# Kernel tuning notes

Measured on AMD Instinct MI355X. Metric: run time of the kernel, lower is better.

The kernel has to match this reference:

```python
import jax, jax.numpy as jnp
import numpy as np

N_NODES = 100000
N_EDGES = 1600000
D = 128
D_FF = 2 * D
BN_EPS = 1e-5


def setup_inputs() -> dict:
    key = jax.random.key(0)
    ks = jax.random.split(key, 16)
    s = lambda k, shp, fan: jax.random.normal(k, shp, jnp.float32) / np.float32(np.sqrt(fan))
    return {
        "x": jax.random.normal(ks[0], (N_NODES, D), jnp.float32),
        "edge_attr": jax.random.normal(ks[1], (N_EDGES, D), jnp.float32),
        "w1g": s(ks[2], (D, D), D),
        "b1g": jnp.zeros((D,), jnp.float32),
        "w2g": s(ks[3], (D, D), D),
        "b2g": jnp.zeros((D,), jnp.float32),
        "bn1_g": jax.random.uniform(ks[4], (D,), jnp.float32, 0.5, 1.5),
        "bn1_b": 0.1 * jax.random.normal(ks[5], (D,), jnp.float32),
        "ff_w1": s(ks[6], (D, D_FF), D),
        "ff_b1": jnp.zeros((D_FF,), jnp.float32),
        "ff_w2": s(ks[7], (D_FF, D), D_FF),
        "ff_b2": jnp.zeros((D,), jnp.float32),
        "bn2_g": jax.random.uniform(ks[8], (D,), jnp.float32, 0.5, 1.5),
        "bn2_b": 0.1 * jax.random.normal(ks[9], (D,), jnp.float32),
        "edge_index": jax.random.randint(ks[10], (2, N_EDGES), 0, N_NODES, jnp.int64 if jax.config.jax_enable_x64 else jnp.int32),
    }


def _batchnorm(h, gamma, beta):
    # training-mode BatchNorm1d: per-batch (node-axis) stats, biased variance
    mean = h.mean(axis=0)
    var = ((h - mean) ** 2).mean(axis=0)
    return gamma * (h - mean) * jax.lax.rsqrt(var + BN_EPS) + beta


def reference(x, edge_attr, w1g, b1g, w2g, b2g, bn1_g, bn1_b,
              ff_w1, ff_b1, ff_w2, ff_b2, bn2_g, bn2_b, edge_index):
    src, dst = edge_index[0], edge_index[1]
    # GINEConv message: relu(x_j + e_ij), scatter-sum into target nodes
    msg = jax.nn.relu(x[src] + edge_attr)                      # [E, D]
    agg = jax.ops.segment_sum(msg, dst, num_segments=N_NODES)  # [N, D]
    h = x + agg                                                # (1+eps)*x with eps=0
    # gin_nn: Linear -> ReLU -> Linear
    h = jax.nn.relu(h @ w1g + b1g) @ w2g + b2g
    h = jax.nn.relu(h)                                         # post-conv relu; dropout=identity (eval)
    h = x + h                                                  # residual
    h = _batchnorm(h, bn1_g, bn1_b)                            # norm1_local
    ff = jax.nn.relu(h @ ff_w1 + ff_b1) @ ff_w2 + ff_b2        # FFN block (dropouts identity)
    h = h + ff
    h = _batchnorm(h, bn2_g, bn2_b)                            # norm2
    return h
```

## Files before the change

### kernel.cpp

```cpp
#include <hip/hip_runtime.h>
#include <hip/hip_bf16.h>

#define NN 100000
#define NE 1600000
#define DD 128
#define DFF 256
#define BN_EPS 1e-5f
#define NND ((size_t)NN * DD)
#define NB_SCAN 391
#define NTILE 6250

typedef __attribute__((ext_vector_type(8))) short short8;
typedef __attribute__((ext_vector_type(4))) float f32x4;
typedef __attribute__((ext_vector_type(4))) unsigned short us4;

static __device__ __forceinline__ unsigned short f2bf(float f) {
  union { float f; unsigned u; } v; v.f = f;
  unsigned r = v.u + 0x7fffu + ((v.u >> 16) & 1u);
  return (unsigned short)(r >> 16);
}
static __device__ __forceinline__ float bf2f(unsigned short h) {
  union { unsigned u; float f; } v; v.u = ((unsigned)h) << 16;
  return v.f;
}

__global__ __launch_bounds__(256) void k_prep_misc(const float* __restrict__ x,
    unsigned short* __restrict__ xbf,
    const float* __restrict__ w1g, const float* __restrict__ w2g,
    const float* __restrict__ ffw1, const float* __restrict__ ffw2,
    unsigned short* __restrict__ w1t, unsigned short* __restrict__ w2t,
    unsigned short* __restrict__ fw1t, unsigned short* __restrict__ fw2t) {
  int b = blockIdx.x;
  if (b < 6250) {
    size_t base = ((size_t)b * 256u + threadIdx.x) * 8;
    const f32x4* xp = reinterpret_cast<const f32x4*>(x + base);
    f32x4 a0 = xp[0], a1 = xp[1];
    short8 o;
#pragma unroll
    for (int j = 0; j < 4; ++j) o[j] = (short)f2bf(a0[j]);
#pragma unroll
    for (int j = 0; j < 4; ++j) o[4 + j] = (short)f2bf(a1[j]);
    *reinterpret_cast<short8*>(xbf + base) = o;
  } else {
    int i = (b - 6250) * 256 + threadIdx.x;
    if (i < 16384) { int c = i & 127, k = i >> 7; w1t[c * 128 + k] = f2bf(w1g[k * 128 + c]); }
    else if (i < 32768) { i -= 16384; int c = i & 127, k = i >> 7; w2t[c * 128 + k] = f2bf(w2g[k * 128 + c]); }
    else if (i < 65536) { i -= 32768; int c = i & 255, k = i >> 8; fw1t[c * 128 + k] = f2bf(ffw1[k * 256 + c]); }
    else if (i < 98304) { i -= 65536; int c = i & 127, k = i >> 7; fw2t[c * 256 + k] = f2bf(ffw2[k * 128 + c]); }
  }
}

__global__ __launch_bounds__(256) void k_hist(const int* __restrict__ ei,
                                              int* __restrict__ cnt) {
  int e = blockIdx.x * 256 + threadIdx.x;
  if (e >= NE) return;
  atomicAdd(&cnt[ei[NE + e]], 1);
}

__global__ __launch_bounds__(256) void k_scan1(const int* __restrict__ cnt,
                                               int* __restrict__ bsum) {
  __shared__ int sh[256];
  int n = blockIdx.x * 256 + threadIdx.x;
  sh[threadIdx.x] = (n < NN) ? cnt[n] : 0;
  __syncthreads();
  for (int off = 128; off > 0; off >>= 1) {
    if (threadIdx.x < off) sh[threadIdx.x] += sh[threadIdx.x + off];
    __syncthreads();
  }
  if (threadIdx.x == 0) bsum[blockIdx.x] = sh[0];
}

__global__ __launch_bounds__(512) void k_scan2(const int* __restrict__ bsum,
                                               int* __restrict__ bpre,
                                               int* __restrict__ rs) {
  __shared__ int sh[512];
  int t = threadIdx.x;
  int v = (t < NB_SCAN) ? bsum[t] : 0;
  sh[t] = v;
  __syncthreads();
  for (int off = 1; off < 512; off <<= 1) {
    int u = (t >= off) ? sh[t - off] : 0;
    __syncthreads();
    sh[t] += u;
    __syncthreads();
  }
  if (t < NB_SCAN) bpre[t] = sh[t] - v;
  if (t == NB_SCAN - 1) rs[NN] = sh[t];
}

__global__ __launch_bounds__(256) void k_scan3(int* __restrict__ rs,
                                               const int* __restrict__ bpre,
                                               int* __restrict__ cursor) {
  __shared__ int sh[256];
  int n = blockIdx.x * 256 + threadIdx.x;
  int t = threadIdx.x;
  int v = (n < NN) ? rs[n] : 0;
  sh[t] = v;
  __syncthreads();
  for (int off = 1; off < 256; off <<= 1) {
    int u = (t >= off) ? sh[t - off] : 0;
    __syncthreads();
    sh[t] += u;
    __syncthreads();
  }
  if (n < NN) {
    int ex = bpre[blockIdx.x] + sh[t] - v;
    rs[n] = ex;
    cursor[n] = ex;
  }
}

__global__ __launch_bounds__(256) void k_scatter(const int* __restrict__ ei,
                                                 int* __restrict__ cursor,
                                                 int2* __restrict__ el2) {
  int e = blockIdx.x * 256 + threadIdx.x;
  if (e >= NE) return;
  int s = ei[e], d = ei[NE + e];
  int p = atomicAdd(&cursor[d], 1);
  el2[p] = make_int2(e, s);
}

__global__ __launch_bounds__(256) void k_gather(
    const unsigned short* __restrict__ xbf, const float* __restrict__ ea,
    const int* __restrict__ rs, const int2* __restrict__ el2,
    unsigned short* __restrict__ h0) {
  int n = blockIdx.x * 8 + (threadIdx.x >> 5);
  int q = threadIdx.x & 31;
  int beg = rs[n], end = rs[n + 1];
  f32x4 acc = (f32x4){0.f, 0.f, 0.f, 0.f};
  int2 E0 = make_int2(0, 0), E1 = E0, E2 = E0, E3 = E0;
  int i = beg;
  if (i     < end) E0 = el2[i];
  if (i + 1 < end) E1 = el2[i + 1];
  if (i + 2 < end) E2 = el2[i + 2];
  if (i + 3 < end) E3 = el2[i + 3];
  for (; i + 4 <= end; i += 4) {
    f32x4 ev0 = *(reinterpret_cast<const f32x4*>(ea + (size_t)E0.x * DD) + q);
    us4  xv0 = *reinterpret_cast<const us4*>(xbf + (size_t)E0.y * DD + q * 4);
    f32x4 ev1 = *(reinterpret_cast<const f32x4*>(ea + (size_t)E1.x * DD) + q);
    us4  xv1 = *reinterpret_cast<const us4*>(xbf + (size_t)E1.y * DD + q * 4);
    f32x4 ev2 = *(reinterpret_cast<const f32x4*>(ea + (size_t)E2.x * DD) + q);
    us4  xv2 = *reinterpret_cast<const us4*>(xbf + (size_t)E2.y * DD + q * 4);
    f32x4 ev3 = *(reinterpret_cast<const f32x4*>(ea + (size_t)E3.x * DD) + q);
    us4  xv3 = *reinterpret_cast<const us4*>(xbf + (size_t)E3.y * DD + q * 4);
    int2 N0 = E0, N1 = E1, N2 = E2, N3 = E3;
    if (i + 4 < end) N0 = el2[i + 4];
    if (i + 5 < end) N1 = el2[i + 5];
    if (i + 6 < end) N2 = el2[i + 6];
    if (i + 7 < end) N3 = el2[i + 7];
#pragma unroll
    for (int c = 0; c < 4; ++c) {
      float m0 = bf2f((unsigned short)xv0[c]) + ev0[c];
      acc[c] += (m0 > 0.f) ? m0 : 0.f;
      float m1 = bf2f((unsigned short)xv1[c]) + ev1[c];
      acc[c] += (m1 > 0.f) ? m1 : 0.f;
      float m2 = bf2f((unsigned short)xv2[c]) + ev2[c];
      acc[c] += (m2 > 0.f) ? m2 : 0.f;
      float m3 = bf2f((unsigned short)xv3[c]) + ev3[c];
      acc[c] += (m3 > 0.f) ? m3 : 0.f;
    }
    E0 = N0; E1 = N1; E2 = N2; E3 = N3;
  }
  if (i < end) {
    f32x4 ev = *(reinterpret_cast<const f32x4*>(ea + (size_t)E0.x * DD) + q);
    us4  xv = *reinterpret_cast<const us4*>(xbf + (size_t)E0.y * DD + q * 4);
#pragma unroll
    for (int c = 0; c < 4; ++c) {
      float m = bf2f((unsigned short)xv[c]) + ev[c];
      acc[c] += (m > 0.f) ? m : 0.f;
    }
  }
  if (i + 1 < end) {
    f32x4 ev = *(reinterpret_cast<const f32x4*>(ea + (size_t)E1.x * DD) + q);
    us4  xv = *reinterpret_cast<const us4*>(xbf + (size_t)E1.y * DD + q * 4);
#pragma unroll
    for (int c = 0; c < 4; ++c) {
      float m = bf2f((unsigned short)xv[c]) + ev[c];
      acc[c] += (m > 0.f) ? m : 0.f;
    }
  }
  if (i + 2 < end) {
    f32x4 ev = *(reinterpret_cast<const f32x4*>(ea + (size_t)E2.x * DD) + q);
    us4  xv = *reinterpret_cast<const us4*>(xbf + (size_t)E2.y * DD + q * 4);
#pragma unroll
    for (int c = 0; c < 4; ++c) {
      float m = bf2f((unsigned short)xv[c]) + ev[c];
      acc[c] += (m > 0.f) ? m : 0.f;
    }
  }
  us4 xs = *reinterpret_cast<const us4*>(xbf + (size_t)n * DD + q * 4);
  union { unsigned short us[4]; unsigned long long u; } pk;
#pragma unroll
  for (int c = 0; c < 4; ++c) pk.us[c] = f2bf(bf2f((unsigned short)xs[c]) + acc[c]);
  *reinterpret_cast<unsigned long long*>(h0 + (size_t)n * DD + q * 4) = pk.u;
}

#define TR1 136
__global__ __launch_bounds__(256) void k_mlp1(const unsigned short* __restrict__ A,
    const unsigned short* __restrict__ W1T, const float* __restrict__ b1,
    const unsigned short* __restrict__ W2T, const float* __restrict__ b2,
    const float* __restrict__ x, float* __restrict__ O, float* __restrict__ stats) {
  __shared__ unsigned short tr[4][16 * TR1];
  __shared__ float lds_s[128], lds_q[128];
  if (threadIdx.x < 128) { lds_s[threadIdx.x] = 0.f; lds_q[threadIdx.x] = 0.f; }
  int lane = threadIdx.x & 63, w = threadIdx.x >> 6;
  int tile = blockIdx.x * 4 + w;
  int l15 = lane & 15, g = lane >> 4;
  int row0 = tile * 16;
  __syncthreads();
  if (tile < NTILE) {
    f32x4 acc[8];
#pragma unroll
    for (int ct = 0; ct < 8; ++ct) {
      float b = b1[ct * 16 + l15];
      acc[ct] = (f32x4){b, b, b, b};
    }
    short8 a[4];
#pragma unroll
    for (int kt = 0; kt < 4; ++kt)
      a[kt] = *reinterpret_cast<const short8*>(A + (size_t)(row0 + l15) * DD + kt * 32 + g * 8);
#pragma unroll
    for (int kt = 0; kt < 4; ++kt) {
      int k0 = kt * 32 + g * 8;
#pragma unroll
      for (int ct = 0; ct < 8; ++ct) {
        int c = ct * 16 + l15;
        short8 b = *reinterpret_cast<const short8*>(W1T + (size_t)c * DD + k0);
        acc[ct] = __builtin_amdgcn_mfma_f32_16x16x32_bf16(a[kt], b, acc[ct], 0, 0, 0);
      }
    }
#pragma unroll
    for (int ct = 0; ct < 8; ++ct) {
#pragma unroll
      for (int r = 0; r < 4; ++r) {
        float v = acc[ct][r];
        v = v > 0.f ? v : 0.f;
        tr[w][(g * 4 + r) * TR1 + ct * 16 + l15] = f2bf(v);
      }
    }
  }
  __syncthreads();
  if (tile < NTILE) {
    short8 a2[4];
#pragma unroll
    for (int kt = 0; kt < 4; ++kt)
      a2[kt] = *reinterpret_cast<const short8*>(&tr[w][l15 * TR1 + kt * 32 + g * 8]);
    f32x4 acc2[8];
#pragma unroll
    for (int ct = 0; ct < 8; ++ct) {
      float b = b2[ct * 16 + l15];
      acc2[ct] = (f32x4){b, b, b, b};
    }
#pragma unroll
    for (int kt = 0; kt < 4; ++kt) {
      int k0 = kt * 32 + g * 8;
#pragma unroll
      for (int ct = 0; ct < 8; ++ct) {
        int c = ct * 16 + l15;
        short8 b = *reinterpret_cast<const short8*>(W2T + (size_t)c * DD + k0);
        acc2[ct] = __builtin_amdgcn_mfma_f32_16x16x32_bf16(a2[kt], b, acc2[ct], 0, 0, 0);
      }
    }
#pragma unroll
    for (int ct = 0; ct < 8; ++ct) {
      int c = ct * 16 + l15;
      float s = 0.f, q = 0.f;
#pragma unroll
      for (int r = 0; r < 4; ++r) {
        int row = row0 + g * 4 + r;
        float v = acc2[ct][r];
        v = v > 0.f ? v : 0.f;
        v += x[(size_t)row * DD + c];
        O[(size_t)row * DD + c] = v;
        s += v; q += v * v;
      }
      s += __shfl_xor(s, 16); s += __shfl_xor(s, 32);
      q += __shfl_xor(q, 16); q += __shfl_xor(q, 32);
      if (g == 0) { atomicAdd(&lds_s[c], s); atomicAdd(&lds_q[c], q); }
    }
  }
  __syncthreads();
  if (threadIdx.x < 128) {
    atomicAdd(&stats[threadIdx.x], lds_s[threadIdx.x]);
    atomicAdd(&stats[128 + threadIdx.x], lds_q[threadIdx.x]);
  }
}

__global__ void k_bnfin(const float* __restrict__ st, const float* __restrict__ gm,
                        const float* __restrict__ bt, float* __restrict__ par) {
  int c = threadIdx.x;
  float mean = st[c] * (1.f / NN);
  float var = st[128 + c] * (1.f / NN) - mean * mean;
  float sc = gm[c] * rsqrtf(var + BN_EPS);
  par[c] = sc;
  par[128 + c] = bt[c] - mean * sc;
}

#define TR2 264
__global__ __launch_bounds__(256) void k_mlp2(const float* __restrict__ H,
    const float* __restrict__ par, const unsigned short* __restrict__ FW1T,
    const float* __restrict__ fb1, const unsigned short* __restrict__ FW2T,
    const float* __restrict__ fb2, float* __restrict__ O, float* __restrict__ stats) {
  __shared__ unsigned short tr[4][16 * TR2];
  __shared__ float lds_s[128], lds_q[128];
  if (threadIdx.x < 128) { lds_s[threadIdx.x] = 0.f; lds_q[threadIdx.x] = 0.f; }
  int lane = threadIdx.x & 63, w = threadIdx.x >> 6;
  int tile = blockIdx.x * 4 + w;
  int l15 = lane & 15, g = lane >> 4;
  int row0 = tile * 16;
  __syncthreads();
  if (tile < NTILE) {
    const float* arow = H + (size_t)(row0 + l15) * DD;
    short8 a1[4];
#pragma unroll
    for (int kt = 0; kt < 4; ++kt) {
      int k0 = kt * 32 + g * 8;
      f32x4 u0 = *reinterpret_cast<const f32x4*>(arow + k0);
      f32x4 u1 = *reinterpret_cast<const f32x4*>(arow + k0 + 4);
      f32x4 sc0 = *reinterpret_cast<const f32x4*>(par + k0);
      f32x4 sc1 = *reinterpret_cast<const f32x4*>(par + k0 + 4);
      f32x4 sh0 = *reinterpret_cast<const f32x4*>(par + 128 + k0);
      f32x4 sh1 = *reinterpret_cast<const f32x4*>(par + 128 + k0 + 4);
      short8 af;
#pragma unroll
      for (int j = 0; j < 4; ++j) af[j] = (short)f2bf(sc0[j] * u0[j] + sh0[j]);
#pragma unroll
      for (int j = 0; j < 4; ++j) af[4 + j] = (short)f2bf(sc1[j] * u1[j] + sh1[j]);
      a1[kt] = af;
    }
    f32x4 acc1[16];
#pragma unroll
    for (int ct = 0; ct < 16; ++ct) {
      float b = fb1[ct * 16 + l15];
      acc1[ct] = (f32x4){b, b, b, b};
    }
#pragma unroll
    for (int kt = 0; kt < 4; ++kt) {
      int k0 = kt * 32 + g * 8;
#pragma unroll
      for (int ct = 0; ct < 16; ++ct) {
        int c = ct * 16 + l15;
        short8 b = *reinterpret_cast<const short8*>(FW1T + (size_t)c * DD + k0);
        acc1[ct] = __builtin_amdgcn_mfma_f32_16x16x32_bf16(a1[kt], b, acc1[ct], 0, 0, 0);
      }
    }
#pragma unroll
    for (int ct = 0; ct < 16; ++ct) {
#pragma unroll
      for (int r = 0; r < 4; ++r) {
        float v = acc1[ct][r];
        v = v > 0.f ? v : 0.f;
        tr[w][(g * 4 + r) * TR2 + ct * 16 + l15] = f2bf(v);
      }
    }
  }
  __syncthreads();
  if (tile < NTILE) {
    short8 a2[8];
#pragma unroll
    for (int kt = 0; kt < 8; ++kt)
      a2[kt] = *reinterpret_cast<const short8*>(&tr[w][l15 * TR2 + kt * 32 + g * 8]);
    f32x4 acc2[8];
#pragma unroll
    for (int ct = 0; ct < 8; ++ct) {
      float b = fb2[ct * 16 + l15];
      acc2[ct] = (f32x4){b, b, b, b};
    }
#pragma unroll 2
    for (int kt = 0; kt < 8; ++kt) {
      int k0 = kt * 32 + g * 8;
#pragma unroll
      for (int ct = 0; ct < 8; ++ct) {
        int c = ct * 16 + l15;
        short8 b = *reinterpret_cast<const short8*>(FW2T + (size_t)c * DFF + k0);
        acc2[ct] = __builtin_amdgcn_mfma_f32_16x16x32_bf16(a2[kt], b, acc2[ct], 0, 0, 0);
      }
    }
#pragma unroll
    for (int ct = 0; ct < 8; ++ct) {
      int c = ct * 16 + l15;
      float sc = par[c], sh = par[128 + c];
      float s = 0.f, q = 0.f;
#pragma unroll
      for (int r = 0; r < 4; ++r) {
        int row = row0 + g * 4 + r;
        float h1v = sc * O[(size_t)row * DD + c] + sh;
        float v = acc2[ct][r] + h1v;
        O[(size_t)row * DD + c] = v;
        s += v; q += v * v;
      }
      s += __shfl_xor(s, 16); s += __shfl_xor(s, 32);
      q += __shfl_xor(q, 16); q += __shfl_xor(q, 32);
      if (g == 0) { atomicAdd(&lds_s[c], s); atomicAdd(&lds_q[c], q); }
    }
  }
  __syncthreads();
  if (threadIdx.x < 128) {
    atomicAdd(&stats[threadIdx.x], lds_s[threadIdx.x]);
    atomicAdd(&stats[128 + threadIdx.x], lds_q[threadIdx.x]);
  }
}

__global__ __launch_bounds__(256) void k_bnfinal(float* __restrict__ h,
    const float* __restrict__ st, const float* __restrict__ gm,
    const float* __restrict__ bt) {
  size_t base = ((size_t)blockIdx.x * 256u + threadIdx.x) * 4;
  int c0 = (int)(base & 127);
  f32x4 v = *reinterpret_cast<f32x4*>(h + base);
#pragma unroll
  for (int j = 0; j < 4; ++j) {
    int c = c0 + j;
    float mean = st[c] * (1.f / NN);
    float var = st[128 + c] * (1.f / NN) - mean * mean;
    float sc = gm[c] * rsqrtf(var + BN_EPS);
    float sh = bt[c] - mean * sc;
    v[j] = sc * v[j] + sh;
  }
  *reinterpret_cast<f32x4*>(h + base) = v;
}

extern "C" void kernel_launch(void* const* d_in, const int* in_sizes, int n_in,
                              void* d_out, int out_size, void* d_ws, size_t ws_size,
                              hipStream_t stream) {
  const float* x    = (const float*)d_in[0];
  const float* ea   = (const float*)d_in[1];
  const float* w1g  = (const float*)d_in[2];
  const float* b1g  = (const float*)d_in[3];
  const float* w2g  = (const float*)d_in[4];
  const float* b2g  = (const float*)d_in[5];
  const float* bn1g = (const float*)d_in[6];
  const float* bn1b = (const float*)d_in[7];
  const float* ffw1 = (const float*)d_in[8];
  const float* ffb1 = (const float*)d_in[9];
  const float* ffw2 = (const float*)d_in[10];
  const float* ffb2 = (const float*)d_in[11];
  const float* bn2g = (const float*)d_in[12];
  const float* bn2b = (const float*)d_in[13];
  const int*   eidx = (const int*)d_in[14];
  float* out = (float*)d_out;

  char* ws = (char*)d_ws;
  int2* el2    = (int2*)(ws);
  int*  rs     = (int*)(ws + 12800000);
  int*  cursor = (int*)(ws + 13200128);
  int*  bsum   = (int*)(ws + 13600128);
  int*  bpre   = (int*)(ws + 13601728);
  float* stats = (float*)(ws + 13603328);
  float* par   = (float*)(ws + 13605376);
  unsigned short* w1t  = (unsigned short*)(ws + 13607424);
  unsigned short* w2t  = w1t + 16384;
  unsigned short* fw1t = w2t + 16384;
  unsigned short* fw2t = fw1t + 32768;
  unsigned short* xbf  = (unsigned short*)(ws + 13804032);
  unsigned short* hbf  = (unsigned short*)(ws + 39404032);

  hipMemsetAsync(rs, 0, (NN + 1) * 4, stream);
  hipMemsetAsync(stats, 0, 512 * 4, stream);

  k_prep_misc<<<6634, 256, 0, stream>>>(x, xbf, w1g, w2g, ffw1, ffw2,
                                        w1t, w2t, fw1t, fw2t);

  k_hist<<<6250, 256, 0, stream>>>(eidx, rs);
  k_scan1<<<NB_SCAN, 256, 0, stream>>>(rs, bsum);
  k_scan2<<<1, 512, 0, stream>>>(bsum, bpre, rs);
  k_scan3<<<NB_SCAN, 256, 0, stream>>>(rs, bpre, cursor);
  k_scatter<<<6250, 256, 0, stream>>>(eidx, cursor, el2);

  k_gather<<<12500, 256, 0, stream>>>(xbf, ea, rs, el2, hbf);

  k_mlp1<<<1563, 256, 0, stream>>>(hbf, w1t, b1g, w2t, b2g, x, out, stats);
  k_bnfin<<<1, 128, 0, stream>>>(stats, bn1g, bn1b, par);
  k_mlp2<<<1563, 256, 0, stream>>>(out, par, fw1t, ffb1, fw2t, ffb2, out, stats + 256);
  k_bnfinal<<<12500, 256, 0, stream>>>(out, stats + 256, bn2g, bn2b);
}
```

Before: 722.0 us.

## Widen gather to one wave per node, fuse histogram, drop memset

The gather kernel now gives each destination node a full 64-lane wave instead of 32 lanes. Each lane handles two features with float2/uint loads, and a double-buffered 4-edge prefetch scheme keeps more loads in flight. The degree histogram is merged into the prep kernel launch, and zeroing of the BN stats moves into the scan2 kernel, which removes a memset. mlp1 now reads the residual from bf16 x instead of fp32 x, cutting residual read bandwidth at a small cost in precision. The narrower per-lane loads may lower memory efficiency per instruction.

Measured after the change: 746.5 us. 1.03x slower.

```diff
diff --git a/kernel.cpp b/kernel.cpp
--- a/kernel.cpp
+++ b/kernel.cpp
@@ -12,7 +12,6 @@
 
 typedef __attribute__((ext_vector_type(8))) short short8;
 typedef __attribute__((ext_vector_type(4))) float f32x4;
-typedef __attribute__((ext_vector_type(4))) unsigned short us4;
 
 static __device__ __forceinline__ unsigned short f2bf(float f) {
   union { float f; unsigned u; } v; v.f = f;
@@ -29,7 +28,8 @@
     const float* __restrict__ w1g, const float* __restrict__ w2g,
     const float* __restrict__ ffw1, const float* __restrict__ ffw2,
     unsigned short* __restrict__ w1t, unsigned short* __restrict__ w2t,
-    unsigned short* __restrict__ fw1t, unsigned short* __restrict__ fw2t) {
+    unsigned short* __restrict__ fw1t, unsigned short* __restrict__ fw2t,
+    const int* __restrict__ ei, int* __restrict__ cnt) {
   int b = blockIdx.x;
   if (b < 6250) {
     size_t base = ((size_t)b * 256u + threadIdx.x) * 8;
@@ -41,20 +41,16 @@
 #pragma unroll
     for (int j = 0; j < 4; ++j) o[4 + j] = (short)f2bf(a1[j]);
     *reinterpret_cast<short8*>(xbf + base) = o;
-  } else {
+  } else if (b < 6634) {
     int i = (b - 6250) * 256 + threadIdx.x;
     if (i < 16384) { int c = i & 127, k = i >> 7; w1t[c * 128 + k] = f2bf(w1g[k * 128 + c]); }
     else if (i < 32768) { i -= 16384; int c = i & 127, k = i >> 7; w2t[c * 128 + k] = f2bf(w2g[k * 128 + c]); }
     else if (i < 65536) { i -= 32768; int c = i & 255, k = i >> 8; fw1t[c * 128 + k] = f2bf(ffw1[k * 256 + c]); }
     else if (i < 98304) { i -= 65536; int c = i & 127, k = i >> 7; fw2t[c * 256 + k] = f2bf(ffw2[k * 128 + c]); }
-  }
-}
-
-__global__ __launch_bounds__(256) void k_hist(const int* __restrict__ ei,
-                                              int* __restrict__ cnt) {
-  int e = blockIdx.x * 256 + threadIdx.x;
-  if (e >= NE) return;
-  atomicAdd(&cnt[ei[NE + e]], 1);
+  } else {
+    int e = (b - 6634) * 256 + threadIdx.x;
+    if (e < NE) atomicAdd(&cnt[ei[NE + e]], 1);
+  }
 }
 
 __global__ __launch_bounds__(256) void k_scan1(const int* __restrict__ cnt,
@@ -72,9 +68,11 @@
 
 __global__ __launch_bounds__(512) void k_scan2(const int* __restrict__ bsum,
                                                int* __restrict__ bpre,
-                                               int* __restrict__ rs) {
+                                               int* __restrict__ rs,
+                                               float* __restrict__ stats) {
   __shared__ int sh[512];
   int t = threadIdx.x;
+  stats[t] = 0.f;
   int v = (t < NB_SCAN) ? bsum[t] : 0;
   sh[t] = v;
   __syncthreads();
@@ -120,86 +118,75 @@
   el2[p] = make_int2(e, s);
 }
 
+#define G_FILL(ix, ev, xv, base)                                               \
+  do {                                                                         \
+    _Pragma("unroll")                                                          \
+    for (int j = 0; j < 4; ++j) {                                              \
+      int pp = (base) + j;                                                     \
+      ix[j] = (pp < end) ? el2[pp] : make_int2(0, 0);                          \
+    }                                                                          \
+    _Pragma("unroll")                                                          \
+    for (int j = 0; j < 4; ++j) {                                              \
+      ev[j] = *reinterpret_cast<const float2*>(ea + (size_t)ix[j].x * DD + 2 * q); \
+      xv[j] = *reinterpret_cast<const unsigned*>(xbf + (size_t)ix[j].y * DD + 2 * q); \
+    }                                                                          \
+  } while (0)
+
+#define G_CONS(ev, xv, cnt)                                                    \
+  do {                                                                         \
+    _Pragma("unroll")                                                          \
+    for (int j = 0; j < 4; ++j) {                                              \
+      if (j < (cnt)) {                                                         \
+        float m0 = bf2f((unsigned short)(xv[j] & 0xffffu)) + ev[j].x;          \
+        float m1 = bf2f((unsigned short)(xv[j] >> 16)) + ev[j].y;              \
+        accx += m0 > 0.f ? m0 : 0.f;                                           \
+        accy += m1 > 0.f ? m1 : 0.f;                                           \
+      }                                                                        \
+    }                                                                          \
+  } while (0)
+
 __global__ __launch_bounds__(256) void k_gather(
     const unsigned short* __restrict__ xbf, const float* __restrict__ ea,
     const int* __restrict__ rs, const int2* __restrict__ el2,
     unsigned short* __restrict__ h0) {
-  int n = blockIdx.x * 8 + (threadIdx.x >> 5);
-  int q = threadIdx.x & 31;
+  int n = blockIdx.x * 4 + (threadIdx.x >> 6);
+  int q = threadIdx.x & 63;
   int beg = rs[n], end = rs[n + 1];
-  f32x4 acc = (f32x4){0.f, 0.f, 0.f, 0.f};
-  int2 E0 = make_int2(0, 0), E1 = E0, E2 = E0, E3 = E0;
-  int i = beg;
-  if (i     < end) E0 = el2[i];
-  if (i + 1 < end) E1 = el2[i + 1];
-  if (i + 2 < end) E2 = el2[i + 2];
-  if (i + 3 < end) E3 = el2[i + 3];
-  for (; i + 4 <= end; i += 4) {
-    f32x4 ev0 = *(reinterpret_cast<const f32x4*>(ea + (size_t)E0.x * DD) + q);
-    us4  xv0 = *reinterpret_cast<const us4*>(xbf + (size_t)E0.y * DD + q * 4);
-    f32x4 ev1 = *(reinterpret_cast<const f32x4*>(ea + (size_t)E1.x * DD) + q);
-    us4  xv1 = *reinterpret_cast<const us4*>(xbf + (size_t)E1.y * DD + q * 4);
-    f32x4 ev2 = *(reinterpret_cast<const f32x4*>(ea + (size_t)E2.x * DD) + q);
-    us4  xv2 = *reinterpret_cast<const us4*>(xbf + (size_t)E2.y * DD + q * 4);
-    f32x4 ev3 = *(reinterpret_cast<const f32x4*>(ea + (size_t)E3.x * DD) + q);
-    us4  xv3 = *reinterpret_cast<const us4*>(xbf + (size_t)E3.y * DD + q * 4);
-    int2 N0 = E0, N1 = E1, N2 = E2, N3 = E3;
-    if (i + 4 < end) N0 = el2[i + 4];
-    if (i + 5 < end) N1 = el2[i + 5];
-    if (i + 6 < end) N2 = el2[i + 6];
-    if (i + 7 < end) N3 = el2[i + 7];
-#pragma unroll
-    for (int c = 0; c < 4; ++c) {
-      float m0 = bf2f((unsigned short)xv0[c]) + ev0[c];
-      acc[c] += (m0 > 0.f) ? m0 : 0.f;
-      float m1 = bf2f((unsigned short)xv1[c]) + ev1[c];
-      acc[c] += (m1 > 0.f) ? m1 : 0.f;
-      float m2 = bf2f((unsigned short)xv2[c]) + ev2[c];
-      acc[c] += (m2 > 0.f) ? m2 : 0.f;
-      float m3 = bf2f((unsigned short)xv3[c]) + ev3[c];
-      acc[c] += (m3 > 0.f) ? m3 : 0.f;
-    }
-    E0 = N0; E1 = N1; E2 = N2; E3 = N3;
-  }
-  if (i < end) {
-    f32x4 ev = *(reinterpret_cast<const f32x4*>(ea + (size_t)E0.x * DD) + q);
-    us4  xv = *reinterpret_cast<const us4*>(xbf + (size_t)E0.y * DD + q * 4);
-#pragma unroll
-    for (int c = 0; c < 4; ++c) {
-      float m = bf2f((unsigned short)xv[c]) + ev[c];
-      acc[c] += (m > 0.f) ? m : 0.f;
-    }
-  }
-  if (i + 1 < end) {
-    f32x4 ev = *(reinterpret_cast<const f32x4*>(ea + (size_t)E1.x * DD) + q);
-    us4  xv = *reinterpret_cast<const us4*>(xbf + (size_t)E1.y * DD + q * 4);
-#pragma unroll
-    for (int c = 0; c < 4; ++c) {
-      float m = bf2f((unsigned short)xv[c]) + ev[c];
-      acc[c] += (m > 0.f) ? m : 0.f;
-    }
-  }
-  if (i + 2 < end) {
-    f32x4 ev = *(reinterpret_cast<const f32x4*>(ea + (size_t)E2.x * DD) + q);
-    us4  xv = *reinterpret_cast<const us4*>(xbf + (size_t)E2.y * DD + q * 4);
-#pragma unroll
-    for (int c = 0; c < 4; ++c) {
-      float m = bf2f((unsigned short)xv[c]) + ev[c];
-      acc[c] += (m > 0.f) ? m : 0.f;
-    }
-  }
-  us4 xs = *reinterpret_cast<const us4*>(xbf + (size_t)n * DD + q * 4);
-  union { unsigned short us[4]; unsigned long long u; } pk;
-#pragma unroll
-  for (int c = 0; c < 4; ++c) pk.us[c] = f2bf(bf2f((unsigned short)xs[c]) + acc[c]);
-  *reinterpret_cast<unsigned long long*>(h0 + (size_t)n * DD + q * 4) = pk.u;
+  int deg = end - beg;
+  float accx = 0.f, accy = 0.f;
+  int nch = (deg + 3) >> 2;
+  if (nch > 0) {
+    int2 ia[4], ib[4];
+    float2 eva[4], evb[4];
+    unsigned xa[4], xb[4];
+    G_FILL(ia, eva, xa, beg);
+    if (nch > 1) G_FILL(ib, evb, xb, beg + 4);
+    for (int c = 0; c < nch; c += 2) {
+      int baseA = beg + c * 4;
+      int cntA = end - baseA; cntA = cntA > 4 ? 4 : cntA;
+      G_CONS(eva, xa, cntA);
+      if (c + 2 < nch) G_FILL(ia, eva, xa, beg + (c + 2) * 4);
+      if (c + 1 < nch) {
+        int baseB = baseA + 4;
+        int cntB = end - baseB; cntB = cntB > 4 ? 4 : cntB;
+        G_CONS(evb, xb, cntB);
+        if (c + 3 < nch) G_FILL(ib, evb, xb, beg + (c + 3) * 4);
+      }
+    }
+  }
+  unsigned xs = *reinterpret_cast<const unsigned*>(xbf + (size_t)n * DD + 2 * q);
+  unsigned short o0 = f2bf(bf2f((unsigned short)(xs & 0xffffu)) + accx);
+  unsigned short o1 = f2bf(bf2f((unsigned short)(xs >> 16)) + accy);
+  *reinterpret_cast<unsigned*>(h0 + (size_t)n * DD + 2 * q) =
+      (unsigned)o0 | ((unsigned)o1 << 16);
 }
 
 #define TR1 136
 __global__ __launch_bounds__(256) void k_mlp1(const unsigned short* __restrict__ A,
     const unsigned short* __restrict__ W1T, const float* __restrict__ b1,
     const unsigned short* __restrict__ W2T, const float* __restrict__ b2,
-    const float* __restrict__ x, float* __restrict__ O, float* __restrict__ stats) {
+    const unsigned short* __restrict__ xbf, float* __restrict__ O,
+    float* __restrict__ stats) {
   __shared__ unsigned short tr[4][16 * TR1];
   __shared__ float lds_s[128], lds_q[128];
   if (threadIdx.x < 128) { lds_s[threadIdx.x] = 0.f; lds_q[threadIdx.x] = 0.f; }
@@ -270,7 +257,7 @@
         int row = row0 + g * 4 + r;
         float v = acc2[ct][r];
         v = v > 0.f ? v : 0.f;
-        v += x[(size_t)row * DD + c];
+        v += bf2f(xbf[(size_t)row * DD + c]);
         O[(size_t)row * DD + c] = v;
         s += v; q += v * v;
       }
@@ -455,20 +442,18 @@
   unsigned short* hbf  = (unsigned short*)(ws + 39404032);
 
   hipMemsetAsync(rs, 0, (NN + 1) * 4, stream);
-  hipMemsetAsync(stats, 0, 512 * 4, stream);
-
-  k_prep_misc<<<6634, 256, 0, stream>>>(x, xbf, w1g, w2g, ffw1, ffw2,
-                                        w1t, w2t, fw1t, fw2t);
-
-  k_hist<<<6250, 256, 0, stream>>>(eidx, rs);
+
+  k_prep_misc<<<12884, 256, 0, stream>>>(x, xbf, w1g, w2g, ffw1, ffw2,
+                                         w1t, w2t, fw1t, fw2t, eidx, rs);
+
   k_scan1<<<NB_SCAN, 256, 0, stream>>>(rs, bsum);
-  k_scan2<<<1, 512, 0, stream>>>(bsum, bpre, rs);
+  k_scan2<<<1, 512, 0, stream>>>(bsum, bpre, rs, stats);
   k_scan3<<<NB_SCAN, 256, 0, stream>>>(rs, bpre, cursor);
   k_scatter<<<6250, 256, 0, stream>>>(eidx, cursor, el2);
 
-  k_gather<<<12500, 256, 0, stream>>>(xbf, ea, rs, el2, hbf);
-
-  k_mlp1<<<1563, 256, 0, stream>>>(hbf, w1t, b1g, w2t, b2g, x, out, stats);
+  k_gather<<<25000, 256, 0, stream>>>(xbf, ea, rs, el2, hbf);
+
+  k_mlp1<<<1563, 256, 0, stream>>>(hbf, w1t, b1g, w2t, b2g, xbf, out, stats);
   k_bnfin<<<1, 128, 0, stream>>>(stats, bn1g, bn1b, par);
   k_mlp2<<<1563, 256, 0, stream>>>(out, par, fw1t, ffb1, fw2t, ffb2, out, stats + 256);
   k_bnfinal<<<12500, 256, 0, stream>>>(out, stats + 256, bn2g, bn2b);
```
